# Kernel optimization log

Hardware: AMD Instinct MI355X
Metric: run time of the kernel (lower is better)

Reference implementation:

```python
import jax, jax.numpy as jnp
import numpy as np

D_MODEL = 1024
NUM_HEADS = 16
MAX_LEN = 500
D_K = D_MODEL // NUM_HEADS


def setup_inputs() -> dict:
    key = jax.random.key(0)
    ks = jax.random.split(key, 10)
    B, L = 8, 500
    s = 1.0 / np.sqrt(D_MODEL)
    return {
        "query": jax.random.normal(ks[0], (B, L, D_MODEL), dtype=jnp.float32),
        "key": jax.random.normal(ks[1], (B, L, D_MODEL), dtype=jnp.float32),
        "value": jax.random.normal(ks[2], (B, L, D_MODEL), dtype=jnp.float32),
        "Wq": jax.random.normal(ks[3], (D_MODEL, D_MODEL), dtype=jnp.float32) * s,
        "bq": jnp.zeros((D_MODEL,), dtype=jnp.float32),
        "Wk": jax.random.normal(ks[4], (D_MODEL, D_MODEL), dtype=jnp.float32) * s,
        "bk": jnp.zeros((D_MODEL,), dtype=jnp.float32),
        "Wv": jax.random.normal(ks[5], (D_MODEL, D_MODEL), dtype=jnp.float32) * s,
        "bv": jnp.zeros((D_MODEL,), dtype=jnp.float32),
        "rel_emb": jax.random.normal(ks[6], (NUM_HEADS, 2 * MAX_LEN - 1), dtype=jnp.float32),
    }


def reference(query, key, value, Wq, bq, Wk, bk, Wv, bv, rel_emb):
    B, Lq, _ = query.shape
    Lk = key.shape[1]
    H, dk = NUM_HEADS, D_K
    # QKV projections -> [B, H, L, d]
    q = (query @ Wq + bq).reshape(B, Lq, H, dk).transpose(0, 2, 1, 3)
    k = (key @ Wk + bk).reshape(B, Lk, H, dk).transpose(0, 2, 1, 3)
    v = (value @ Wv + bv).reshape(B, Lk, H, dk).transpose(0, 2, 1, 3)
    scores = jnp.einsum('bhqd,bhkd->bhqk', q, k) / jnp.sqrt(jnp.float32(dk))
    # gathered relative-position bias: [H, Lq, Lk]
    rel_idx = jnp.arange(Lq)[:, None] - jnp.arange(Lk)[None, :] + MAX_LEN - 1
    bias = rel_emb[:, rel_idx]  # [H, Lq, Lk]
    scores = scores + bias[None]
    attn = jax.nn.softmax(scores, axis=-1)
    out = jnp.einsum('bhqk,bhkd->bhqd', attn, v)
    return out.transpose(0, 2, 1, 3).reshape(B, Lq, H * dk)
```

## Files before the change

### kernel.cpp

```cpp
#include <hip/hip_runtime.h>

typedef short bf16x8 __attribute__((ext_vector_type(8)));
typedef float f32x4 __attribute__((ext_vector_type(4)));
typedef unsigned uint4v __attribute__((ext_vector_type(4)));

#define B_    8
#define L_    500
#define LP    512
#define H_    16
#define DK    64
#define DM    1024
#define MP    4096
#define NT    8

static __device__ __forceinline__ unsigned short f2bf(float x) {
  unsigned u = __float_as_uint(x);
  u += 0x7fffu + ((u >> 16) & 1u);
  return (unsigned short)(u >> 16);
}

static __device__ __forceinline__ unsigned cvtpk(float lo, float hi) {
  unsigned r;
  asm("v_cvt_pk_bf16_f32 %0, %1, %2" : "=v"(r) : "v"(lo), "v"(hi));
  return r;
}

static __device__ __forceinline__ void gload16(const void* g, void* l) {
  __builtin_amdgcn_global_load_lds(
      (const __attribute__((address_space(1))) void*)g,
      (__attribute__((address_space(3))) void*)l, 16, 0, 0);
}

static __device__ __forceinline__ f32x4 MF(bf16x8 a, bf16x8 b, f32x4 c) {
  return __builtin_amdgcn_mfma_f32_16x16x32_bf16(a, b, c, 0, 0, 0);
}

__global__ __launch_bounds__(256) void conv_kernel(
    const float* __restrict__ iq, const float* __restrict__ ik,
    const float* __restrict__ iv,
    const float* __restrict__ wq, const float* __restrict__ wk,
    const float* __restrict__ wv,
    unsigned short* __restrict__ X, unsigned short* __restrict__ Wt,
    unsigned short* __restrict__ vt) {
  const int z = blockIdx.y;
  const int bx = blockIdx.x;
  const int tid = threadIdx.x;
  if (bx < 2048) {
    const float* src = (z == 0) ? iq : (z == 1) ? ik : iv;
    const size_t off = ((size_t)bx * 256 + tid) * 8;
    const int m = (int)(off >> 10);
    unsigned short o[8];
    if (m < 4000) {
      const float4 a = *(const float4*)(src + off);
      const float4 b = *(const float4*)(src + off + 4);
      o[0]=f2bf(a.x); o[1]=f2bf(a.y); o[2]=f2bf(a.z); o[3]=f2bf(a.w);
      o[4]=f2bf(b.x); o[5]=f2bf(b.y); o[6]=f2bf(b.z); o[7]=f2bf(b.w);
    } else {
#pragma unroll
      for (int i = 0; i < 8; ++i) o[i] = 0;
    }
    uint4 pk;
    pk.x = (unsigned)o[0] | ((unsigned)o[1] << 16);
    pk.y = (unsigned)o[2] | ((unsigned)o[3] << 16);
    pk.z = (unsigned)o[4] | ((unsigned)o[5] << 16);
    pk.w = (unsigned)o[6] | ((unsigned)o[7] << 16);
    *(uint4*)(X + (size_t)z * MP * DM + off) = pk;
    return;
  }
  if (bx >= 2304) {
    if (z == 0) {
      const int idx = (bx - 2304) * 256 + tid;
      unsigned short* p = vt + (size_t)idx * LP + 496;
      const uint4 zz = {0u, 0u, 0u, 0u};
      *(uint4*)(p)     = zz;
      *(uint4*)(p + 8) = zz;
    }
    return;
  }
  const int bw = bx - 2048;
  const float* W = (z == 0) ? wq : (z == 1) ? wk : wv;
  const int k0 = (bw >> 4) * 64;
  const int n0 = (bw & 15) * 64;
  __shared__ float t[64][65];
  const int row = tid >> 2;
  const int cb  = (tid & 3) * 16;
#pragma unroll
  for (int s = 0; s < 4; ++s) {
    const float4 v = *(const float4*)(W + (size_t)(k0 + row) * DM + n0 + cb + s * 4);
    t[row][cb + s * 4 + 0] = v.x; t[row][cb + s * 4 + 1] = v.y;
    t[row][cb + s * 4 + 2] = v.z; t[row][cb + s * 4 + 3] = v.w;
  }
  __syncthreads();
  const int nr = tid >> 2;
  const int kb = (tid & 3) * 16;
#pragma unroll
  for (int s = 0; s < 2; ++s) {
    unsigned short o[8];
#pragma unroll
    for (int e = 0; e < 8; ++e) o[e] = f2bf(t[kb + s * 8 + e][nr]);
    uint4 pk;
    pk.x = (unsigned)o[0] | ((unsigned)o[1] << 16);
    pk.y = (unsigned)o[2] | ((unsigned)o[3] << 16);
    pk.z = (unsigned)o[4] | ((unsigned)o[5] << 16);
    pk.w = (unsigned)o[6] | ((unsigned)o[7] << 16);
    *(uint4*)(Wt + (size_t)z * DM * DM + (size_t)(n0 + nr) * DM + k0 + kb + s * 8) = pk;
  }
}

__global__ __launch_bounds__(256) void gemm_qkv_kernel(
    const unsigned short* __restrict__ X, const unsigned short* __restrict__ Wt,
    const float* __restrict__ bq, const float* __restrict__ bk,
    const float* __restrict__ bv,
    unsigned short* __restrict__ qo, unsigned short* __restrict__ ko,
    unsigned short* __restrict__ vo) {
  const int z = blockIdx.y;
  const unsigned short* A  = X  + (size_t)z * MP * DM;
  const unsigned short* Bw = Wt + (size_t)z * DM * DM;
  const float* bias = (z == 0) ? bq : (z == 1) ? bk : bv;
  unsigned short* out = (z == 0) ? qo : (z == 1) ? ko : vo;

  const int bid = blockIdx.x;
  const int xg = bid & 7, y = bid >> 3;
  const int tm = xg + 8 * (y >> 3);
  const int tn = y & 7;
  const int tid = threadIdx.x;
  const int lane = tid & 63, wid = tid >> 6;
  const int wr = wid >> 1, wc = wid & 1;
  const int lg = lane >> 4, lr = lane & 15;

  __shared__ __attribute__((aligned(16))) unsigned short sA[3][128 * 32];
  __shared__ __attribute__((aligned(16))) unsigned short sB[3][128 * 32];

  const int c0 = tid, c1 = tid + 256;
  const int ar0 = c0 >> 2, ak0 = (c0 & 3) * 8;
  const int ar1 = c1 >> 2, ak1 = (c1 & 3) * 8;
  const unsigned short* Ab = A  + (size_t)tm * 128 * DM;
  const unsigned short* Bb = Bw + (size_t)tn * 128 * DM;

  auto STAGE = [&](int t) {
    const int buf = t % 3;
    const int kn = t * 32;
    gload16(Ab + (size_t)ar0 * DM + kn + ak0, &sA[buf][c0 * 8]);
    gload16(Ab + (size_t)ar1 * DM + kn + ak1, &sA[buf][c1 * 8]);
    gload16(Bb + (size_t)ar0 * DM + kn + ak0, &sB[buf][c0 * 8]);
    gload16(Bb + (size_t)ar1 * DM + kn + ak1, &sB[buf][c1 * 8]);
  };

  f32x4 acc[4][4];
#pragma unroll
  for (int i = 0; i < 4; ++i)
#pragma unroll
    for (int j = 0; j < 4; ++j) acc[i][j] = (f32x4){0.f, 0.f, 0.f, 0.f};

  STAGE(0); STAGE(1);
  asm volatile("s_waitcnt vmcnt(4)" ::: "memory");
  __builtin_amdgcn_s_barrier();
  __builtin_amdgcn_sched_barrier(0);

  for (int t = 0; t < 32; ++t) {
    if (t < 30) STAGE(t + 2);
    const int cb = t % 3;
    bf16x8 af[4], bfr[4];
#pragma unroll
    for (int s = 0; s < 4; ++s) {
      af[s]  = *(const bf16x8*)&sA[cb][(wr * 64 + s * 16 + lr) * 32 + lg * 8];
      bfr[s] = *(const bf16x8*)&sB[cb][(wc * 64 + s * 16 + lr) * 32 + lg * 8];
    }
#pragma unroll
    for (int i = 0; i < 4; ++i)
#pragma unroll
      for (int j = 0; j < 4; ++j)
        acc[i][j] = MF(af[i], bfr[j], acc[i][j]);
    if (t < 31) {
      if (t < 30) asm volatile("s_waitcnt vmcnt(4)" ::: "memory");
      else        asm volatile("s_waitcnt vmcnt(0)" ::: "memory");
      __builtin_amdgcn_s_barrier();
      __builtin_amdgcn_sched_barrier(0);
    }
  }

  const int nbase = tn * 128 + wc * 64 + lr;
  float bias4[4];
#pragma unroll
  for (int ns = 0; ns < 4; ++ns) bias4[ns] = bias[nbase + ns * 16];

  if (z == 2) {
    unsigned short* T = (wid == 0) ? &sA[0][0] : (wid == 1) ? &sA[2][0]
                      : (wid == 2) ? &sB[0][0] : &sB[2][0];
    const int hh = tn * 2 + wc;
    const int m0w = tm * 128 + wr * 64;
    const int li = lane & 15;
    const int m = m0w + li * 4;
    const unsigned batch = (unsigned)m / 500u;
    const int lrow = m - (int)batch * 500;
    unsigned short* ob = out + (((size_t)batch * H_ + hh) * DK) * LP + lrow;
    const bool ok = (m < 4000);
#pragma unroll
    for (int half = 0; half < 2; ++half) {
#pragma unroll
      for (int ms = 0; ms < 4; ++ms)
#pragma unroll
        for (int nsl = 0; nsl < 2; ++nsl) {
          const int ns = half * 2 + nsl;
          uint2 pk;
          pk.x = (unsigned)f2bf(acc[ms][ns][0] + bias4[ns]) |
                 ((unsigned)f2bf(acc[ms][ns][1] + bias4[ns]) << 16);
          pk.y = (unsigned)f2bf(acc[ms][ns][2] + bias4[ns]) |
                 ((unsigned)f2bf(acc[ms][ns][3] + bias4[ns]) << 16);
          *(uint2*)&T[(nsl * 16 + lr) * 72 + ms * 16 + lg * 4] = pk;
        }
      asm volatile("s_waitcnt lgkmcnt(0)" ::: "memory");
      __builtin_amdgcn_sched_barrier(0);
      if (ok) {
#pragma unroll
        for (int it = 0; it < 8; ++it) {
          const int dl = it * 4 + lg;
          const uint2 v = *(const uint2*)&T[dl * 72 + li * 4];
          *(uint2*)(ob + (size_t)(half * 32 + dl) * LP) = v;
        }
      }
      asm volatile("s_waitcnt lgkmcnt(0)" ::: "memory");
      __builtin_amdgcn_sched_barrier(0);
    }
  } else {
#pragma unroll
    for (int ms = 0; ms < 4; ++ms) {
#pragma unroll
      for (int r = 0; r < 4; ++r) {
        const int m = tm * 128 + wr * 64 + ms * 16 + lg * 4 + r;
        if (m < 4000) {
          const unsigned batch = (unsigned)m / 500u;
          const int lrow = m - (int)batch * 500;
#pragma unroll
          for (int ns = 0; ns < 4; ++ns) {
            const int n = nbase + ns * 16;
            const int hh = n >> 6, d = n & 63;
            out[(((size_t)batch * H_ + hh) * LP + lrow) * DK + d] =
                f2bf(acc[ms][ns][r] + bias4[ns]);
          }
        }
      }
    }
  }
}

__global__ __launch_bounds__(512, 2) void attn_kernel(
    const unsigned short* __restrict__ q, const unsigned short* __restrict__ k,
    const unsigned short* __restrict__ vt, const float* __restrict__ rel,
    float* __restrict__ out) {
  const int id = blockIdx.x;
  const int bh = id & 127, qc = id >> 7;
  const int b = bh >> 4, h = bh & 15;
  const int tid = threadIdx.x;
  const int lane = tid & 63, wid = tid >> 6;
  const int lg = lane >> 4, lr = lane & 15;

  __shared__ unsigned short kt[2][2][64][32];
  __shared__ unsigned short vtt[2][2][64][32];
  __shared__ float relb[640];

  const float LOG2E = 1.44269504f;
  const float SC = 0.125f * LOG2E;
  const int rbase = qc * 128 - 12;
  for (int i = tid; i < 639; i += 512) {
    int idx = rbase + i;
    idx = idx < 0 ? 0 : (idx > 998 ? 998 : idx);
    relb[i] = rel[h * 999 + idx] * LOG2E;
  }

  const int qrow = qc * 128 + wid * 16 + lr;
  const unsigned short* qp = q + ((size_t)bh * LP + qrow) * DK + lg * 8;
  const bf16x8 qf0 = *(const bf16x8*)qp;
  const bf16x8 qf1 = *(const bf16x8*)(qp + 32);

  const int kj = tid >> 3, dcs = (tid & 7) * 8;
  const unsigned short* kgp = k + ((size_t)bh * LP + kj) * DK + dcs;
  unsigned short* kls = &kt[0][dcs >> 5][kj][dcs & 31];
  const int vd = tid >> 3, vkg = (tid & 7) * 8;
  const unsigned short* vgp = vt + ((size_t)bh * DK + vd) * LP + vkg;
  unsigned short* vls = &vtt[0][vkg >> 5][vd][vkg & 31];

  const int sig0 = 8 * (lr >> 2) + (lr & 3);
  const int qin = wid * 16 + lr;

  f32x4 o[4];
#pragma unroll
  for (int d = 0; d < 4; ++d) o[d] = (f32x4){0.f, 0.f, 0.f, 0.f};
  float mrun = -1e30f, lrun = 0.f;

  uint4 ka0 = *(const uint4*)(kgp);
  uint4 va0 = *(const uint4*)(vgp);

  for (int t = 0; t < NT; ++t) {
    const int buf = t & 1;
    *(uint4*)(kls + buf * 4096) = ka0;
    *(uint4*)(vls + buf * 4096) = va0;
    __syncthreads();

    if (t < NT - 1) {
      ka0 = *(const uint4*)(kgp + (size_t)(t + 1) * 64 * DK);
      va0 = *(const uint4*)(vgp + (t + 1) * 64);
    }

    f32x4 s[2][2];
#pragma unroll
    for (int kc = 0; kc < 2; ++kc)
#pragma unroll
      for (int hf = 0; hf < 2; ++hf) {
        const int sg = kc * 32 + hf * 4 + sig0;
        const bf16x8 a0 = *(const bf16x8*)&kt[buf][0][sg][lg * 8];
        const bf16x8 a1 = *(const bf16x8*)&kt[buf][1][sg][lg * 8];
        f32x4 ss = (f32x4){0.f, 0.f, 0.f, 0.f};
        ss = __builtin_amdgcn_mfma_f32_16x16x32_bf16(a0, qf0, ss, 0, 0, 0);
        ss = __builtin_amdgcn_mfma_f32_16x16x32_bf16(a1, qf1, ss, 0, 0, 0);
        s[kc][hf] = ss;
      }

    float sc[2][2][4];
#pragma unroll
    for (int kc = 0; kc < 2; ++kc)
#pragma unroll
      for (int hf = 0; hf < 2; ++hf) {
        const int bidx = qin - (t * 64 + kc * 32 + 8 * lg + 4 * hf) + 511;
#pragma unroll
        for (int r = 0; r < 4; ++r)
          sc[kc][hf][r] = s[kc][hf][r] * SC + relb[bidx - r];
      }
    if (t == NT - 1) {
#pragma unroll
      for (int hf = 0; hf < 2; ++hf)
#pragma unroll
        for (int r = 0; r < 4; ++r)
          if (8 * lg + 4 * hf + r >= 20) sc[1][hf][r] = -1e30f;
    }

    float m0 = fmaxf(fmaxf(sc[0][0][0], sc[0][0][1]), fmaxf(sc[0][0][2], sc[0][0][3]));
    float m1 = fmaxf(fmaxf(sc[0][1][0], sc[0][1][1]), fmaxf(sc[0][1][2], sc[0][1][3]));
    float m2 = fmaxf(fmaxf(sc[1][0][0], sc[1][0][1]), fmaxf(sc[1][0][2], sc[1][0][3]));
    float m3 = fmaxf(fmaxf(sc[1][1][0], sc[1][1][1]), fmaxf(sc[1][1][2], sc[1][1][3]));
    const float mloc = fmaxf(fmaxf(m0, m1), fmaxf(m2, m3));
    if (!__all(mloc - mrun <= 11.5f)) {
      float mx = fmaxf(mloc, mrun);
      mx = fmaxf(mx, __shfl_xor(mx, 16));
      mx = fmaxf(mx, __shfl_xor(mx, 32));
      const float alpha = exp2f(mrun - mx);
      mrun = mx;
      lrun *= alpha;
#pragma unroll
      for (int d = 0; d < 4; ++d) {
        o[d][0] *= alpha; o[d][1] *= alpha; o[d][2] *= alpha; o[d][3] *= alpha;
      }
    }

    float rs = 0.f;
    unsigned pw[2][4];
#pragma unroll
    for (int kc = 0; kc < 2; ++kc)
#pragma unroll
      for (int hf = 0; hf < 2; ++hf) {
        float p0 = exp2f(sc[kc][hf][0] - mrun);
        float p1 = exp2f(sc[kc][hf][1] - mrun);
        float p2 = exp2f(sc[kc][hf][2] - mrun);
        float p3 = exp2f(sc[kc][hf][3] - mrun);
        rs += (p0 + p1) + (p2 + p3);
        pw[kc][hf * 2 + 0] = cvtpk(p0, p1);
        pw[kc][hf * 2 + 1] = cvtpk(p2, p3);
      }
    rs += __shfl_xor(rs, 16);
    rs += __shfl_xor(rs, 32);
    lrun += rs;

#pragma unroll
    for (int kc = 0; kc < 2; ++kc) {
      union { uint4v u; bf16x8 v; } cv;
      cv.u = (uint4v){pw[kc][0], pw[kc][1], pw[kc][2], pw[kc][3]};
      const bf16x8 pf = cv.v;
#pragma unroll
      for (int db = 0; db < 4; ++db) {
        const bf16x8 vf = *(const bf16x8*)&vtt[buf][kc][db * 16 + lr][lg * 8];
        o[db] = __builtin_amdgcn_mfma_f32_16x16x32_bf16(vf, pf, o[db], 0, 0, 0);
      }
    }
  }

  if (qrow < L_) {
    const float inv = 1.0f / lrun;
    float* op = out + ((size_t)b * L_ + qrow) * DM + h * DK + lg * 4;
#pragma unroll
    for (int db = 0; db < 4; ++db) {
      float4 v;
      v.x = o[db][0] * inv; v.y = o[db][1] * inv;
      v.z = o[db][2] * inv; v.w = o[db][3] * inv;
      *(float4*)(op + db * 16) = v;
    }
  }
}

extern "C" void kernel_launch(void* const* d_in, const int* in_sizes, int n_in,
                              void* d_out, int out_size, void* d_ws, size_t ws_size,
                              hipStream_t stream) {
  const float* iq  = (const float*)d_in[0];
  const float* ik  = (const float*)d_in[1];
  const float* iv  = (const float*)d_in[2];
  const float* wq  = (const float*)d_in[3];
  const float* bq  = (const float*)d_in[4];
  const float* wk  = (const float*)d_in[5];
  const float* bk  = (const float*)d_in[6];
  const float* wv  = (const float*)d_in[7];
  const float* bv  = (const float*)d_in[8];
  const float* rel = (const float*)d_in[9];
  float* out = (float*)d_out;

  char* w = (char*)d_ws;
  unsigned short* X   = (unsigned short*)(w);
  unsigned short* Wt  = (unsigned short*)(w + 25165824);
  unsigned short* qb  = (unsigned short*)(w + 31457280);
  unsigned short* kb  = (unsigned short*)(w + 39845888);
  unsigned short* vtb = (unsigned short*)(w + 48234496);

  conv_kernel<<<dim3(2336, 3), 256, 0, stream>>>(iq, ik, iv, wq, wk, wv, X, Wt, vtb);
  gemm_qkv_kernel<<<dim3(256, 3), 256, 0, stream>>>(X, Wt, bq, bk, bv, qb, kb, vtb);
  attn_kernel<<<512, 512, 0, stream>>>(qb, kb, vtb, rel, out);
}
```

Measured before the change: 83.28 us.

## Fuse fp32-to-bf16 activation conversion into QKV GEMM A-tile loads

Drops the separate pass that converted the query/key/value activations to a padded bf16 buffer. The GEMM now loads fp32 rows directly into registers, zero-fills rows past 4000, packs them to bf16 with v_cvt_pk_bf16_f32, and writes them to a double-buffered LDS A tile. The B tile keeps its triple-buffered direct-to-LDS path, and the V-output transpose epilogue is reworked to fit the smaller LDS. This removes a full write-and-reread of the activations, but the A path now goes through registers and the GEMM reads twice as many bytes for A, which could stall the MFMA loop.

After: 222.7 us. +167.4%, slower.

```diff
diff --git a/kernel.cpp b/kernel.cpp
--- a/kernel.cpp
+++ b/kernel.cpp
@@ -10,7 +10,6 @@
 #define H_    16
 #define DK    64
 #define DM    1024
-#define MP    4096
 #define NT    8
 
 static __device__ __forceinline__ unsigned short f2bf(float x) {
@@ -36,40 +35,15 @@
 }
 
 __global__ __launch_bounds__(256) void conv_kernel(
-    const float* __restrict__ iq, const float* __restrict__ ik,
-    const float* __restrict__ iv,
     const float* __restrict__ wq, const float* __restrict__ wk,
     const float* __restrict__ wv,
-    unsigned short* __restrict__ X, unsigned short* __restrict__ Wt,
-    unsigned short* __restrict__ vt) {
+    unsigned short* __restrict__ Wt, unsigned short* __restrict__ vt) {
   const int z = blockIdx.y;
   const int bx = blockIdx.x;
   const int tid = threadIdx.x;
-  if (bx < 2048) {
-    const float* src = (z == 0) ? iq : (z == 1) ? ik : iv;
-    const size_t off = ((size_t)bx * 256 + tid) * 8;
-    const int m = (int)(off >> 10);
-    unsigned short o[8];
-    if (m < 4000) {
-      const float4 a = *(const float4*)(src + off);
-      const float4 b = *(const float4*)(src + off + 4);
-      o[0]=f2bf(a.x); o[1]=f2bf(a.y); o[2]=f2bf(a.z); o[3]=f2bf(a.w);
-      o[4]=f2bf(b.x); o[5]=f2bf(b.y); o[6]=f2bf(b.z); o[7]=f2bf(b.w);
-    } else {
-#pragma unroll
-      for (int i = 0; i < 8; ++i) o[i] = 0;
-    }
-    uint4 pk;
-    pk.x = (unsigned)o[0] | ((unsigned)o[1] << 16);
-    pk.y = (unsigned)o[2] | ((unsigned)o[3] << 16);
-    pk.z = (unsigned)o[4] | ((unsigned)o[5] << 16);
-    pk.w = (unsigned)o[6] | ((unsigned)o[7] << 16);
-    *(uint4*)(X + (size_t)z * MP * DM + off) = pk;
-    return;
-  }
-  if (bx >= 2304) {
+  if (bx >= 256) {
     if (z == 0) {
-      const int idx = (bx - 2304) * 256 + tid;
+      const int idx = (bx - 256) * 256 + tid;
       unsigned short* p = vt + (size_t)idx * LP + 496;
       const uint4 zz = {0u, 0u, 0u, 0u};
       *(uint4*)(p)     = zz;
@@ -77,10 +51,9 @@
     }
     return;
   }
-  const int bw = bx - 2048;
   const float* W = (z == 0) ? wq : (z == 1) ? wk : wv;
-  const int k0 = (bw >> 4) * 64;
-  const int n0 = (bw & 15) * 64;
+  const int k0 = (bx >> 4) * 64;
+  const int n0 = (bx & 15) * 64;
   __shared__ float t[64][65];
   const int row = tid >> 2;
   const int cb  = (tid & 3) * 16;
@@ -108,13 +81,14 @@
 }
 
 __global__ __launch_bounds__(256) void gemm_qkv_kernel(
-    const unsigned short* __restrict__ X, const unsigned short* __restrict__ Wt,
+    const float* __restrict__ xq, const float* __restrict__ xk,
+    const float* __restrict__ xv, const unsigned short* __restrict__ Wt,
     const float* __restrict__ bq, const float* __restrict__ bk,
     const float* __restrict__ bv,
     unsigned short* __restrict__ qo, unsigned short* __restrict__ ko,
     unsigned short* __restrict__ vo) {
   const int z = blockIdx.y;
-  const unsigned short* A  = X  + (size_t)z * MP * DM;
+  const float* Af = (z == 0) ? xq : (z == 1) ? xk : xv;
   const unsigned short* Bw = Wt + (size_t)z * DM * DM;
   const float* bias = (z == 0) ? bq : (z == 1) ? bk : bv;
   unsigned short* out = (z == 0) ? qo : (z == 1) ? ko : vo;
@@ -128,22 +102,43 @@
   const int wr = wid >> 1, wc = wid & 1;
   const int lg = lane >> 4, lr = lane & 15;
 
-  __shared__ __attribute__((aligned(16))) unsigned short sA[3][128 * 32];
+  __shared__ __attribute__((aligned(16))) unsigned short sA[2][128 * 32];
   __shared__ __attribute__((aligned(16))) unsigned short sB[3][128 * 32];
 
   const int c0 = tid, c1 = tid + 256;
   const int ar0 = c0 >> 2, ak0 = (c0 & 3) * 8;
   const int ar1 = c1 >> 2, ak1 = (c1 & 3) * 8;
-  const unsigned short* Ab = A  + (size_t)tm * 128 * DM;
+  const int am0 = tm * 128 + ar0, am1 = tm * 128 + ar1;
+  const bool ok0 = am0 < 4000, ok1 = am1 < 4000;
+  const float* fA0 = Af + (size_t)am0 * DM + ak0;
+  const float* fA1 = Af + (size_t)am1 * DM + ak1;
   const unsigned short* Bb = Bw + (size_t)tn * 128 * DM;
-
-  auto STAGE = [&](int t) {
+  const unsigned short* gB0 = Bb + (size_t)ar0 * DM + ak0;
+  const unsigned short* gB1 = Bb + (size_t)ar1 * DM + ak1;
+
+  float4 r0, r1, r2, r3;
+  const float4 fz = {0.f, 0.f, 0.f, 0.f};
+  auto LOADA = [&](int t) {
+    const int kn = t * 32;
+    if (ok0) { r0 = *(const float4*)(fA0 + kn); r1 = *(const float4*)(fA0 + kn + 4); }
+    else     { r0 = fz; r1 = fz; }
+    if (ok1) { r2 = *(const float4*)(fA1 + kn); r3 = *(const float4*)(fA1 + kn + 4); }
+    else     { r2 = fz; r3 = fz; }
+  };
+  auto WRITEA = [&](int buf) {
+    uint4 w0, w1;
+    w0.x = cvtpk(r0.x, r0.y); w0.y = cvtpk(r0.z, r0.w);
+    w0.z = cvtpk(r1.x, r1.y); w0.w = cvtpk(r1.z, r1.w);
+    w1.x = cvtpk(r2.x, r2.y); w1.y = cvtpk(r2.z, r2.w);
+    w1.z = cvtpk(r3.x, r3.y); w1.w = cvtpk(r3.z, r3.w);
+    *(uint4*)&sA[buf][c0 * 8] = w0;
+    *(uint4*)&sA[buf][c1 * 8] = w1;
+  };
+  auto STAGEB = [&](int t) {
     const int buf = t % 3;
     const int kn = t * 32;
-    gload16(Ab + (size_t)ar0 * DM + kn + ak0, &sA[buf][c0 * 8]);
-    gload16(Ab + (size_t)ar1 * DM + kn + ak1, &sA[buf][c1 * 8]);
-    gload16(Bb + (size_t)ar0 * DM + kn + ak0, &sB[buf][c0 * 8]);
-    gload16(Bb + (size_t)ar1 * DM + kn + ak1, &sB[buf][c1 * 8]);
+    gload16(gB0 + kn, &sB[buf][c0 * 8]);
+    gload16(gB1 + kn, &sB[buf][c1 * 8]);
   };
 
   f32x4 acc[4][4];
@@ -152,18 +147,22 @@
 #pragma unroll
     for (int j = 0; j < 4; ++j) acc[i][j] = (f32x4){0.f, 0.f, 0.f, 0.f};
 
-  STAGE(0); STAGE(1);
-  asm volatile("s_waitcnt vmcnt(4)" ::: "memory");
+  LOADA(0);
+  STAGEB(0); STAGEB(1);
+  WRITEA(0);
+  LOADA(1);
+  asm volatile("s_waitcnt vmcnt(6) lgkmcnt(0)" ::: "memory");
   __builtin_amdgcn_s_barrier();
   __builtin_amdgcn_sched_barrier(0);
 
   for (int t = 0; t < 32; ++t) {
-    if (t < 30) STAGE(t + 2);
+    if (t < 31) WRITEA((t + 1) & 1);
+    if (t < 30) { LOADA(t + 2); STAGEB(t + 2); }
     const int cb = t % 3;
     bf16x8 af[4], bfr[4];
 #pragma unroll
     for (int s = 0; s < 4; ++s) {
-      af[s]  = *(const bf16x8*)&sA[cb][(wr * 64 + s * 16 + lr) * 32 + lg * 8];
+      af[s]  = *(const bf16x8*)&sA[t & 1][(wr * 64 + s * 16 + lr) * 32 + lg * 8];
       bfr[s] = *(const bf16x8*)&sB[cb][(wc * 64 + s * 16 + lr) * 32 + lg * 8];
     }
 #pragma unroll
@@ -172,8 +171,8 @@
       for (int j = 0; j < 4; ++j)
         acc[i][j] = MF(af[i], bfr[j], acc[i][j]);
     if (t < 31) {
-      if (t < 30) asm volatile("s_waitcnt vmcnt(4)" ::: "memory");
-      else        asm volatile("s_waitcnt vmcnt(0)" ::: "memory");
+      if (t < 30) asm volatile("s_waitcnt vmcnt(6) lgkmcnt(0)" ::: "memory");
+      else        asm volatile("s_waitcnt vmcnt(0) lgkmcnt(0)" ::: "memory");
       __builtin_amdgcn_s_barrier();
       __builtin_amdgcn_sched_barrier(0);
     }
@@ -185,7 +184,7 @@
   for (int ns = 0; ns < 4; ++ns) bias4[ns] = bias[nbase + ns * 16];
 
   if (z == 2) {
-    unsigned short* T = (wid == 0) ? &sA[0][0] : (wid == 1) ? &sA[2][0]
+    unsigned short* T = (wid == 0) ? &sA[0][0] : (wid == 1) ? &sA[0][2048]
                       : (wid == 2) ? &sB[0][0] : &sB[2][0];
     const int hh = tn * 2 + wc;
     const int m0w = tm * 128 + wr * 64;
@@ -196,27 +195,24 @@
     unsigned short* ob = out + (((size_t)batch * H_ + hh) * DK) * LP + lrow;
     const bool ok = (m < 4000);
 #pragma unroll
-    for (int half = 0; half < 2; ++half) {
-#pragma unroll
-      for (int ms = 0; ms < 4; ++ms)
-#pragma unroll
-        for (int nsl = 0; nsl < 2; ++nsl) {
-          const int ns = half * 2 + nsl;
-          uint2 pk;
-          pk.x = (unsigned)f2bf(acc[ms][ns][0] + bias4[ns]) |
-                 ((unsigned)f2bf(acc[ms][ns][1] + bias4[ns]) << 16);
-          pk.y = (unsigned)f2bf(acc[ms][ns][2] + bias4[ns]) |
-                 ((unsigned)f2bf(acc[ms][ns][3] + bias4[ns]) << 16);
-          *(uint2*)&T[(nsl * 16 + lr) * 72 + ms * 16 + lg * 4] = pk;
-        }
+    for (int ns = 0; ns < 4; ++ns) {
+#pragma unroll
+      for (int ms = 0; ms < 4; ++ms) {
+        uint2 pk;
+        pk.x = (unsigned)f2bf(acc[ms][ns][0] + bias4[ns]) |
+               ((unsigned)f2bf(acc[ms][ns][1] + bias4[ns]) << 16);
+        pk.y = (unsigned)f2bf(acc[ms][ns][2] + bias4[ns]) |
+               ((unsigned)f2bf(acc[ms][ns][3] + bias4[ns]) << 16);
+        *(uint2*)&T[lr * 72 + ms * 16 + lg * 4] = pk;
+      }
       asm volatile("s_waitcnt lgkmcnt(0)" ::: "memory");
       __builtin_amdgcn_sched_barrier(0);
       if (ok) {
 #pragma unroll
-        for (int it = 0; it < 8; ++it) {
+        for (int it = 0; it < 4; ++it) {
           const int dl = it * 4 + lg;
           const uint2 v = *(const uint2*)&T[dl * 72 + li * 4];
-          *(uint2*)(ob + (size_t)(half * 32 + dl) * LP) = v;
+          *(uint2*)(ob + (size_t)(ns * 16 + dl) * LP) = v;
         }
       }
       asm volatile("s_waitcnt lgkmcnt(0)" ::: "memory");
@@ -412,13 +408,12 @@
   float* out = (float*)d_out;
 
   char* w = (char*)d_ws;
-  unsigned short* X   = (unsigned short*)(w);
   unsigned short* Wt  = (unsigned short*)(w + 25165824);
   unsigned short* qb  = (unsigned short*)(w + 31457280);
   unsigned short* kb  = (unsigned short*)(w + 39845888);
   unsigned short* vtb = (unsigned short*)(w + 48234496);
 
-  conv_kernel<<<dim3(2336, 3), 256, 0, stream>>>(iq, ik, iv, wq, wk, wv, X, Wt, vtb);
-  gemm_qkv_kernel<<<dim3(256, 3), 256, 0, stream>>>(X, Wt, bq, bk, bv, qb, kb, vtb);
+  conv_kernel<<<dim3(288, 3), 256, 0, stream>>>(wq, wk, wv, Wt, vtb);
+  gemm_qkv_kernel<<<dim3(256, 3), 256, 0, stream>>>(iq, ik, iv, Wt, bq, bk, bv, qb, kb, vtb);
   attn_kernel<<<512, 512, 0, stream>>>(qb, kb, vtb, rel, out);
 }
```

## Rewrite QKV GEMM with 256x256 tiles, swizzled LDS and ping-pong MFMA schedule

Applied to the files above, without the earlier changes.

The QKV projection GEMM moves from 128x128 tiles with 256 threads to 256x256 tiles with 512 threads (8 waves, each owning 128x64). The K step grows to 64, the LDS layout uses an XOR swizzle to avoid bank conflicts, and the main loop interleaves global loads with quadrant MFMA groups under barriers and s_setprio. Larger tiles raise data reuse per byte loaded from memory. The cost is only 192 blocks (fewer than the CU count), more register and LDS pressure, and many more barriers per iteration.

Measured after the change: 77.77 us. -6.6%, faster.

```diff
diff --git a/kernel.cpp b/kernel.cpp
--- a/kernel.cpp
+++ b/kernel.cpp
@@ -107,7 +107,29 @@
   }
 }
 
-__global__ __launch_bounds__(256) void gemm_qkv_kernel(
+#define BAR()   __builtin_amdgcn_s_barrier()
+#define LGKM0() do { asm volatile("s_waitcnt lgkmcnt(0)" ::: "memory"); \
+                     __builtin_amdgcn_sched_barrier(0); } while (0)
+#define P1()    __builtin_amdgcn_s_setprio(1)
+#define P0()    __builtin_amdgcn_s_setprio(0)
+
+#define QUAD(AF, BF, MB, NB)                                                   \
+  _Pragma("unroll") for (int mi = 0; mi < 4; ++mi)                             \
+  _Pragma("unroll") for (int ni = 0; ni < 2; ++ni) {                           \
+    acc[(MB)+mi][(NB)+ni] = MF(AF[mi][0], BF[ni][0], acc[(MB)+mi][(NB)+ni]);   \
+    acc[(MB)+mi][(NB)+ni] = MF(AF[mi][1], BF[ni][1], acc[(MB)+mi][(NB)+ni]); }
+
+#define RDAF(P, MQ)                                                            \
+  _Pragma("unroll") for (int mi = 0; mi < 4; ++mi) {                           \
+    af[mi][0] = *(const bf16x8*)&(P)[((MQ)+mi)*1024 + kof0];                   \
+    af[mi][1] = *(const bf16x8*)&(P)[((MQ)+mi)*1024 + kof1]; }
+
+#define RDBF(P, NQ, DST)                                                       \
+  _Pragma("unroll") for (int ni = 0; ni < 2; ++ni) {                           \
+    DST[ni][0] = *(const bf16x8*)&(P)[((NQ)+ni)*1024 + kof0];                  \
+    DST[ni][1] = *(const bf16x8*)&(P)[((NQ)+ni)*1024 + kof1]; }
+
+__global__ __launch_bounds__(512, 2) void gemm_qkv_kernel(
     const unsigned short* __restrict__ X, const unsigned short* __restrict__ Wt,
     const float* __restrict__ bq, const float* __restrict__ bk,
     const float* __restrict__ bv,
@@ -119,104 +141,123 @@
   const float* bias = (z == 0) ? bq : (z == 1) ? bk : bv;
   unsigned short* out = (z == 0) ? qo : (z == 1) ? ko : vo;
 
-  const int bid = blockIdx.x;
-  const int xg = bid & 7, y = bid >> 3;
-  const int tm = xg + 8 * (y >> 3);
-  const int tn = y & 7;
+  const int bx = blockIdx.x;
+  const int xg = bx & 7, y = bx >> 3;
+  const int tm = xg + 8 * (y & 1);
+  const int tn = y >> 1;
+
   const int tid = threadIdx.x;
   const int lane = tid & 63, wid = tid >> 6;
-  const int wr = wid >> 1, wc = wid & 1;
+  const int wr = wid >> 2, wcol = wid & 3;
   const int lg = lane >> 4, lr = lane & 15;
 
-  __shared__ __attribute__((aligned(16))) unsigned short sA[3][128 * 32];
-  __shared__ __attribute__((aligned(16))) unsigned short sB[3][128 * 32];
-
-  const int c0 = tid, c1 = tid + 256;
-  const int ar0 = c0 >> 2, ak0 = (c0 & 3) * 8;
-  const int ar1 = c1 >> 2, ak1 = (c1 & 3) * 8;
-  const unsigned short* Ab = A  + (size_t)tm * 128 * DM;
-  const unsigned short* Bb = Bw + (size_t)tn * 128 * DM;
-
-  auto STAGE = [&](int t) {
-    const int buf = t % 3;
-    const int kn = t * 32;
-    gload16(Ab + (size_t)ar0 * DM + kn + ak0, &sA[buf][c0 * 8]);
-    gload16(Ab + (size_t)ar1 * DM + kn + ak1, &sA[buf][c1 * 8]);
-    gload16(Bb + (size_t)ar0 * DM + kn + ak0, &sB[buf][c0 * 8]);
-    gload16(Bb + (size_t)ar1 * DM + kn + ak1, &sB[buf][c1 * 8]);
+  __shared__ __attribute__((aligned(16))) unsigned short sA[32768];
+  __shared__ __attribute__((aligned(16))) unsigned short sB[32768];
+
+  const int rr = (tid >> 3) & 63;
+  const int g  = tid & 7;
+  const int gx = g ^ (rr & 7);
+  const unsigned short* aSrc = A  + (size_t)(tm * 256 + rr) * DM + gx * 8;
+  const int rb0 = rr + (rr & 32);
+  const unsigned short* bSrc = Bw + (size_t)(tn * 256 + rb0) * DM + gx * 8;
+  const int aD = rr * 64 + g * 8;
+  const int bD = rb0 * 64 + g * 8;
+
+  auto SA_ = [&](int d, int q, int kt) {
+    gload16(aSrc + (size_t)(q * 64) * DM + kt * 64,         &sA[(d*2+0)*8192 + q*4096 + aD]);
+    gload16(aSrc + (size_t)(128 + q * 64) * DM + kt * 64,   &sA[(d*2+1)*8192 + q*4096 + aD]);
   };
-
-  f32x4 acc[4][4];
-#pragma unroll
-  for (int i = 0; i < 4; ++i)
-#pragma unroll
-    for (int j = 0; j < 4; ++j) acc[i][j] = (f32x4){0.f, 0.f, 0.f, 0.f};
-
-  STAGE(0); STAGE(1);
-  asm volatile("s_waitcnt vmcnt(4)" ::: "memory");
-  __builtin_amdgcn_s_barrier();
+  auto SB_ = [&](int d, int q, int kt) {
+    gload16(bSrc + (size_t)(q * 32) * DM + kt * 64,         &sB[(d*2+0)*8192 + q*2048 + bD]);
+    gload16(bSrc + (size_t)(128 + q * 32) * DM + kt * 64,   &sB[(d*2+1)*8192 + q*2048 + bD]);
+  };
+
+  const int kof0 = ((lg)     ^ (lr & 7)) * 8;
+  const int kof1 = ((4 + lg) ^ (lr & 7)) * 8;
+  const unsigned short* pA0 = &sA[(0*2 + wr) * 8192 + lr * 64];
+  const unsigned short* pA1 = &sA[(1*2 + wr) * 8192 + lr * 64];
+  const unsigned short* pB0 = &sB[(0*2 + (wcol >> 1)) * 8192 + (wcol & 1) * 4096 + lr * 64];
+  const unsigned short* pB1 = &sB[(1*2 + (wcol >> 1)) * 8192 + (wcol & 1) * 4096 + lr * 64];
+
+  f32x4 acc[8][4];
+#pragma unroll
+  for (int i = 0; i < 8; ++i)
+#pragma unroll
+    for (int jj = 0; jj < 4; ++jj) acc[i][jj] = (f32x4){0.f, 0.f, 0.f, 0.f};
+
+  SA_(0, 0, 0); SB_(0, 0, 0); SA_(0, 1, 0); SB_(0, 1, 0);
+  SA_(1, 0, 1); SB_(1, 0, 1); SA_(1, 1, 1);
+  asm volatile("s_waitcnt vmcnt(6)" ::: "memory");
+  BAR();
   __builtin_amdgcn_sched_barrier(0);
 
-  for (int t = 0; t < 32; ++t) {
-    if (t < 30) STAGE(t + 2);
-    const int cb = t % 3;
-    bf16x8 af[4], bfr[4];
-#pragma unroll
-    for (int s = 0; s < 4; ++s) {
-      af[s]  = *(const bf16x8*)&sA[cb][(wr * 64 + s * 16 + lr) * 32 + lg * 8];
-      bfr[s] = *(const bf16x8*)&sB[cb][(wc * 64 + s * 16 + lr) * 32 + lg * 8];
-    }
-#pragma unroll
-    for (int i = 0; i < 4; ++i)
-#pragma unroll
-      for (int j = 0; j < 4; ++j)
-        acc[i][j] = MF(af[i], bfr[j], acc[i][j]);
-    if (t < 31) {
-      if (t < 30) asm volatile("s_waitcnt vmcnt(4)" ::: "memory");
-      else        asm volatile("s_waitcnt vmcnt(0)" ::: "memory");
-      __builtin_amdgcn_s_barrier();
-      __builtin_amdgcn_sched_barrier(0);
-    }
-  }
-
-  const int nbase = tn * 128 + wc * 64 + lr;
+  bf16x8 af[4][2], b0[2][2], b1[2][2];
+
+  for (int j = 0; j < 8; ++j) {
+    const int k1 = 2*j + 1, k2 = 2*j + 2, k3 = 2*j + 3;
+    const bool st = (j < 7);
+    RDAF(pA0, 0); RDBF(pB0, 0, b0);
+    SB_(1, 1, k1);
+    BAR(); LGKM0(); P1(); QUAD(af, b0, 0, 0); P0(); BAR();
+    RDBF(pB0, 2, b1);
+    if (st) SA_(0, 0, k2);
+    BAR(); LGKM0(); P1(); QUAD(af, b1, 0, 2); P0(); BAR();
+    RDAF(pA0, 4);
+    if (st) SB_(0, 0, k2);
+    BAR(); LGKM0(); P1(); QUAD(af, b1, 4, 2); P0(); BAR();
+    if (st) SA_(0, 1, k2);
+    BAR(); LGKM0(); P1(); QUAD(af, b0, 4, 0); P0();
+    if (st) asm volatile("s_waitcnt vmcnt(6)" ::: "memory");
+    else    asm volatile("s_waitcnt vmcnt(0)" ::: "memory");
+    BAR();
+    RDAF(pA1, 0); RDBF(pB1, 0, b0);
+    if (st) SB_(0, 1, k2);
+    BAR(); LGKM0(); P1(); QUAD(af, b0, 0, 0); P0(); BAR();
+    RDBF(pB1, 2, b1);
+    if (st) SA_(1, 0, k3);
+    BAR(); LGKM0(); P1(); QUAD(af, b1, 0, 2); P0(); BAR();
+    RDAF(pA1, 4);
+    if (st) SB_(1, 0, k3);
+    BAR(); LGKM0(); P1(); QUAD(af, b1, 4, 2); P0(); BAR();
+    if (st) SA_(1, 1, k3);
+    BAR(); LGKM0(); P1(); QUAD(af, b0, 4, 0); P0();
+    if (st) asm volatile("s_waitcnt vmcnt(6)" ::: "memory");
+    BAR();
+  }
+
+  const int nb = tn * 256 + wcol * 64 + lr;
+  const int hh = tn * 4 + wcol;
   float bias4[4];
 #pragma unroll
-  for (int ns = 0; ns < 4; ++ns) bias4[ns] = bias[nbase + ns * 16];
+  for (int ni = 0; ni < 4; ++ni) bias4[ni] = bias[nb + ni * 16];
 
   if (z == 2) {
-    unsigned short* T = (wid == 0) ? &sA[0][0] : (wid == 1) ? &sA[2][0]
-                      : (wid == 2) ? &sB[0][0] : &sB[2][0];
-    const int hh = tn * 2 + wc;
-    const int m0w = tm * 128 + wr * 64;
-    const int li = lane & 15;
-    const int m = m0w + li * 4;
+    unsigned short* T = sA + wid * 2176;
+    const int li = lane & 31, dsel = lane >> 5;
+    const int m = tm * 256 + wr * 128 + li * 4;
     const unsigned batch = (unsigned)m / 500u;
     const int lrow = m - (int)batch * 500;
+    const bool ok = (m < 4000);
     unsigned short* ob = out + (((size_t)batch * H_ + hh) * DK) * LP + lrow;
-    const bool ok = (m < 4000);
-#pragma unroll
-    for (int half = 0; half < 2; ++half) {
-#pragma unroll
-      for (int ms = 0; ms < 4; ++ms)
-#pragma unroll
-        for (int nsl = 0; nsl < 2; ++nsl) {
-          const int ns = half * 2 + nsl;
-          uint2 pk;
-          pk.x = (unsigned)f2bf(acc[ms][ns][0] + bias4[ns]) |
-                 ((unsigned)f2bf(acc[ms][ns][1] + bias4[ns]) << 16);
-          pk.y = (unsigned)f2bf(acc[ms][ns][2] + bias4[ns]) |
-                 ((unsigned)f2bf(acc[ms][ns][3] + bias4[ns]) << 16);
-          *(uint2*)&T[(nsl * 16 + lr) * 72 + ms * 16 + lg * 4] = pk;
-        }
+#pragma unroll
+    for (int ni = 0; ni < 4; ++ni) {
+#pragma unroll
+      for (int mi = 0; mi < 8; ++mi) {
+        uint2 pk;
+        pk.x = (unsigned)f2bf(acc[mi][ni][0] + bias4[ni]) |
+               ((unsigned)f2bf(acc[mi][ni][1] + bias4[ni]) << 16);
+        pk.y = (unsigned)f2bf(acc[mi][ni][2] + bias4[ni]) |
+               ((unsigned)f2bf(acc[mi][ni][3] + bias4[ni]) << 16);
+        *(uint2*)&T[lr * 136 + mi * 16 + lg * 4] = pk;
+      }
       asm volatile("s_waitcnt lgkmcnt(0)" ::: "memory");
       __builtin_amdgcn_sched_barrier(0);
       if (ok) {
 #pragma unroll
         for (int it = 0; it < 8; ++it) {
-          const int dl = it * 4 + lg;
-          const uint2 v = *(const uint2*)&T[dl * 72 + li * 4];
-          *(uint2*)(ob + (size_t)(half * 32 + dl) * LP) = v;
+          const int dl = it * 2 + dsel;
+          const uint2 v = *(const uint2*)&T[dl * 136 + li * 4];
+          *(uint2*)(ob + (size_t)(ni * 16 + dl) * LP) = v;
         }
       }
       asm volatile("s_waitcnt lgkmcnt(0)" ::: "memory");
@@ -224,20 +265,17 @@
     }
   } else {
 #pragma unroll
-    for (int ms = 0; ms < 4; ++ms) {
+    for (int mi = 0; mi < 8; ++mi) {
 #pragma unroll
       for (int r = 0; r < 4; ++r) {
-        const int m = tm * 128 + wr * 64 + ms * 16 + lg * 4 + r;
+        const int m = tm * 256 + wr * 128 + mi * 16 + lg * 4 + r;
         if (m < 4000) {
           const unsigned batch = (unsigned)m / 500u;
           const int lrow = m - (int)batch * 500;
-#pragma unroll
-          for (int ns = 0; ns < 4; ++ns) {
-            const int n = nbase + ns * 16;
-            const int hh = n >> 6, d = n & 63;
-            out[(((size_t)batch * H_ + hh) * LP + lrow) * DK + d] =
-                f2bf(acc[ms][ns][r] + bias4[ns]);
-          }
+          unsigned short* op = out + (((size_t)batch * H_ + hh) * LP + lrow) * DK + lr;
+#pragma unroll
+          for (int ni = 0; ni < 4; ++ni)
+            op[ni * 16] = f2bf(acc[mi][ni][r] + bias4[ni]);
         }
       }
     }
@@ -419,6 +457,6 @@
   unsigned short* vtb = (unsigned short*)(w + 48234496);
 
   conv_kernel<<<dim3(2336, 3), 256, 0, stream>>>(iq, ik, iv, wq, wk, wv, X, Wt, vtb);
-  gemm_qkv_kernel<<<dim3(256, 3), 256, 0, stream>>>(X, Wt, bq, bk, bv, qb, kb, vtb);
+  gemm_qkv_kernel<<<dim3(64, 3), 512, 0, stream>>>(X, Wt, bq, bk, bv, qb, kb, vtb);
   attn_kernel<<<512, 512, 0, stream>>>(qb, kb, vtb, rel, out);
 }
```
